# Kernel tuning notes

Hardware: AMD Instinct MI355X
Metric: run time of the kernel (lower is better)

Reference implementation:

```python
import jax, jax.numpy as jnp
import numpy as np

NUM_FEATURES = 256   # 2**8
BOND_DIM = 16
N_CORES = 8          # log2(NUM_FEATURES)
BATCH = 262144


def _mpo_cores(mpo_weights, n, bond_dim):
    # Slice the flat parameter vector into n cores of shape (l, r, 2, 2).
    shapes = [(1, bond_dim, 2, 2)] + [(bond_dim, bond_dim, 2, 2)] * (n - 2) + [(bond_dim, 1, 2, 2)]
    cores, off = [], 0
    for s in shapes:
        sz = int(np.prod(s))
        cores.append(mpo_weights[off:off + sz].reshape(s))
        off += sz
    return cores


def _contract_mpo(cores):
    # Sequentially contract the tensor-train cores into the full (2^n, 2^n) matrix.
    # T has axes (bond, I, J) where I/J accumulate the row/col physical bits
    # in order i1..in / j1..jn, matching the original einsum + reshape.
    T = cores[0][0]          # (r, 2, 2)
    dim = 2
    for A in cores[1:]:      # A: (l, r2, 2, 2)
        T = jnp.einsum('aIJ,abkm->bIkJm', T, A).reshape(A.shape[1], dim * 2, dim * 2)
        dim *= 2
    return T[0]              # (2^n, 2^n)


def setup_inputs() -> dict:
    key = jax.random.key(0)
    k1, k2, k3 = jax.random.split(key, 3)
    total = 2 * 4 * BOND_DIM + (N_CORES - 2) * 4 * BOND_DIM ** 2  # 6272
    return {
        'x': jax.random.normal(k1, (BATCH, NUM_FEATURES), dtype=jnp.float32),
        'mpo_weights': jax.random.normal(k2, (total,), dtype=jnp.float32) * 0.1,
        'dense_kernel': jax.random.normal(k3, (NUM_FEATURES, 1), dtype=jnp.float32) * 0.1,
        'dense_bias': jnp.zeros((1,), dtype=jnp.float32),
    }


def reference(x, mpo_weights, dense_kernel, dense_bias):
    W = _contract_mpo(_mpo_cores(mpo_weights, N_CORES, BOND_DIM))  # (256, 256)
    h = jnp.square(x @ W)                                          # (B, 256)
    return h @ dense_kernel + dense_bias                           # (B, 1)
```

## Files before the change

kernel.cpp:

```cpp
#include <hip/hip_runtime.h>
#include <hip/hip_bf16.h>

typedef _Float16 half8 __attribute__((ext_vector_type(8)));
typedef float    floatx4 __attribute__((ext_vector_type(4)));

#define WSCALE      4096.0f
#define WSCALE_INV  (1.0f/(4096.0f*4096.0f))

#define T1_OFF   0
#define U_OFF    4096
#define WF16_OFF 8192

__global__ __launch_bounds__(256)
void mpo_prep1(const float* __restrict__ w, float* __restrict__ ws) {
    __shared__ __align__(16) float wL[3136];
    __shared__ __align__(16) float sL[4352];
    const int tid = threadIdx.x;

    {
        const floatx4* s4 = reinterpret_cast<const floatx4*>(w + blockIdx.x * 3136);
        floatx4* d4 = reinterpret_cast<floatx4*>(wL);
        for (int i = tid; i < 784; i += 256) d4[i] = s4[i];
    }
    __syncthreads();

    if (blockIdx.x == 0) {
        {
            int li = tid;
            int mm = li & 3, kk = (li >> 2) & 3, c = li >> 4;
            int k1 = kk >> 1, k2 = kk & 1, m1 = mm >> 1, m2 = mm & 1;
            float s = 0.f;
#pragma unroll
            for (int b = 0; b < 16; ++b)
                s += wL[b * 4 + k1 * 2 + m1] * wL[64 + b * 64 + c * 4 + k2 * 2 + m2];
            sL[li] = s;
        }
        {
            const int i0 = (tid >> 4) * 4, j0 = (tid & 15) * 4;
            const float* Ab = wL + 1088 + (i0 >> 2) * 64;
            const float* Bb = wL + 2112 + j0;
            float acc[4][4] = {};
#pragma unroll
            for (int b = 0; b < 16; ++b) {
                floatx4 ar = *reinterpret_cast<const floatx4*>(Ab + b * 4);
                floatx4 br = *reinterpret_cast<const floatx4*>(Bb + b * 64);
#pragma unroll
                for (int r = 0; r < 4; ++r)
#pragma unroll
                    for (int s = 0; s < 4; ++s) acc[r][s] += ar[r] * br[s];
            }
#pragma unroll
            for (int r = 0; r < 4; ++r)
#pragma unroll
            for (int s = 0; s < 4; ++s) {
                int i = i0 + r, j = j0 + s;
                sL[256 + (i >> 2) * 256 + (j >> 2) * 16 +
                   ((i >> 1) & 1) * 8 + ((j >> 1) & 1) * 4 + (i & 1) * 2 + (j & 1)] = acc[r][s];
            }
        }
        __syncthreads();
        {
            const int p0 = (tid >> 6) * 4, q0 = (tid & 63) * 4;
            float acc[4][4] = {};
#pragma unroll
            for (int a = 0; a < 16; ++a) {
                floatx4 pr = *reinterpret_cast<const floatx4*>(sL + a * 16 + p0);
                floatx4 qr = *reinterpret_cast<const floatx4*>(sL + 256 + a * 256 + q0);
#pragma unroll
                for (int r = 0; r < 4; ++r)
#pragma unroll
                    for (int s = 0; s < 4; ++s) acc[r][s] += pr[r] * qr[s];
            }
#pragma unroll
            for (int r = 0; r < 4; ++r)
#pragma unroll
            for (int s = 0; s < 4; ++s) {
                int p = p0 + r, q = q0 + s;
                ws[T1_OFF + (q >> 4) * 256 + ((p >> 2) * 4 + ((q >> 2) & 3)) * 16 +
                   (p & 3) * 4 + (q & 3)] = acc[r][s];
            }
        }
    } else {
        {
            const int i0 = (tid >> 4) * 4, j0 = (tid & 15) * 4;
            const float* Ab = wL + (i0 >> 2) * 64;
            const float* Bb = wL + 1024 + j0;
            float acc[4][4] = {};
#pragma unroll
            for (int b = 0; b < 16; ++b) {
                floatx4 ar = *reinterpret_cast<const floatx4*>(Ab + b * 4);
                floatx4 br = *reinterpret_cast<const floatx4*>(Bb + b * 64);
#pragma unroll
                for (int r = 0; r < 4; ++r)
#pragma unroll
                    for (int s = 0; s < 4; ++s) acc[r][s] += ar[r] * br[s];
            }
#pragma unroll
            for (int r = 0; r < 4; ++r)
#pragma unroll
            for (int s = 0; s < 4; ++s) {
                int i = i0 + r, j = j0 + s;
                sL[(i >> 2) * 256 + (j >> 2) * 16 +
                   ((i >> 1) & 1) * 8 + ((j >> 1) & 1) * 4 + (i & 1) * 2 + (j & 1)] = acc[r][s];
            }
        }
        {
            int li = tid;
            int mm = li & 3, kk = (li >> 2) & 3, a = li >> 4;
            int k1 = kk >> 1, k2 = kk & 1, m1 = mm >> 1, m2 = mm & 1;
            float s = 0.f;
#pragma unroll
            for (int b = 0; b < 16; ++b)
                s += wL[2048 + a * 64 + b * 4 + k1 * 2 + m1] * wL[3072 + b * 4 + k2 * 2 + m2];
            sL[4096 + li] = s;
        }
        __syncthreads();
        {
            const int r0 = (tid >> 2) * 4, q0 = (tid & 3) * 4;
            float acc[4][4] = {};
#pragma unroll
            for (int b = 0; b < 16; ++b) {
                floatx4 ar = *reinterpret_cast<const floatx4*>(sL + (r0 >> 4) * 256 + b * 16 + (r0 & 15));
                floatx4 br = *reinterpret_cast<const floatx4*>(sL + 4096 + b * 16 + q0);
#pragma unroll
                for (int r = 0; r < 4; ++r)
#pragma unroll
                    for (int s = 0; s < 4; ++s) acc[r][s] += ar[r] * br[s];
            }
#pragma unroll
            for (int r = 0; r < 4; ++r)
#pragma unroll
            for (int s = 0; s < 4; ++s)
                ws[U_OFF + (r0 + r) * 16 + q0 + s] = acc[r][s];
        }
    }
}

__global__ __launch_bounds__(256)
void mpo_prep2(const float* __restrict__ ws, _Float16* __restrict__ Wf) {
    int idx = blockIdx.x * blockDim.x + threadIdx.x;
    int J4 = idx & 255, I4 = idx >> 8;
    int I16 = I4 >> 4, kc = (I4 >> 2) & 3, k2 = I4 & 3;
    int J16 = J4 >> 4, mc = (J4 >> 2) & 3, m2 = J4 & 3;
    const float* T1 = ws + T1_OFF;
    const float* U  = ws + U_OFF + (((kc * 4 + mc) * 4 + k2) * 4 + m2);
    float s = 0.f;
#pragma unroll
    for (int a = 0; a < 16; ++a)
        s += T1[(a * 16 + I16) * 16 + J16] * U[a * 256];
    int n = J4 >> 4, lr = J4 & 15, kk = I4 >> 5, gg = (I4 >> 3) & 3, j = I4 & 7;
    Wf[(((n * 8 + kk) * 64) + gg * 16 + lr) * 8 + j] = (_Float16)(s * WSCALE);
}

__global__ __launch_bounds__(512, 2)
void mpo_main(const float* __restrict__ x, const _Float16* __restrict__ Wf,
              const float* __restrict__ dk, const float* __restrict__ bias,
              float* __restrict__ out) {
    extern __shared__ _Float16 Wl[];
    float* dkL = reinterpret_cast<float*>(Wl + 65536);

    const int tid  = threadIdx.x;
    const int lane = tid & 63;
    const int wave = tid >> 6;
    const int lrow = lane & 15;
    const int g    = lane >> 4;

    const long blockbase = (long)blockIdx.x * 1024;
    const float* xb = x + (blockbase + wave * 32 + lrow) * 256 + g * 8;
    const int PASS_STRIDE = 256 * 256;
    const int SET_STRIDE  = 16 * 256;

    half8 a0[8], a1[8];
    floatx4 lo[8], hi[8];

#define SB()  __builtin_amdgcn_sched_barrier(0)
#define XLD(i, xn) do { const float* p_ = (xn) + (i) * 32;              \
                     lo[i] = *reinterpret_cast<const floatx4*>(p_);     \
                     hi[i] = *reinterpret_cast<const floatx4*>(p_ + 4); } while (0)
#define XLD_ALL(xn) do { XLD(0,xn); XLD(1,xn); XLD(2,xn); XLD(3,xn); \
                         XLD(4,xn); XLD(5,xn); XLD(6,xn); XLD(7,xn); } while (0)
#define XCVT(dst, i) do { half8 f_;                                           \
                     f_[0] = (_Float16)lo[i][0]; f_[1] = (_Float16)lo[i][1];  \
                     f_[2] = (_Float16)lo[i][2]; f_[3] = (_Float16)lo[i][3];  \
                     f_[4] = (_Float16)hi[i][0]; f_[5] = (_Float16)hi[i][1];  \
                     f_[6] = (_Float16)hi[i][2]; f_[7] = (_Float16)hi[i][3];  \
                     dst[i] = f_; } while (0)
#define XCVT_ALL(dst) do { XCVT(dst,0); XCVT(dst,1); XCVT(dst,2); XCVT(dst,3); \
                           XCVT(dst,4); XCVT(dst,5); XCVT(dst,6); XCVT(dst,7); } while (0)

    XLD_ALL(xb);
    SB();
    {
        const floatx4* src = reinterpret_cast<const floatx4*>(Wf);
        floatx4* dst = reinterpret_cast<floatx4*>(Wl);
#pragma unroll
        for (int i = 0; i < 16; ++i)
            dst[tid + i * 512] = src[tid + i * 512];
    }
    if (tid < 256) dkL[tid] = dk[tid];
    const float bs = bias[0];
    __syncthreads();
    XCVT_ALL(a0);
    XLD_ALL(xb + SET_STRIDE);
    SB();
    XCVT_ALL(a1);
    SB();

    const half8* Wv = reinterpret_cast<const half8*>(Wl);

#pragma unroll 1
    for (int p = 0; p < 4; ++p) {
        if (p < 3) { XLD_ALL(xb + (p + 1) * PASS_STRIDE); }
        SB();

        float rp0[4] = {0, 0, 0, 0}, rp1[4] = {0, 0, 0, 0};
#pragma unroll 1
        for (int n = 0; n < 16; ++n) {
            const float kv = dkL[n * 16 + lrow];
            const half8* Wn = Wv + n * 512 + lane;
            floatx4 c0 = {0, 0, 0, 0}, c1 = {0, 0, 0, 0};
#pragma unroll
            for (int kk = 0; kk < 8; ++kk) {
                half8 b = Wn[kk * 64];
                c0 = __builtin_amdgcn_mfma_f32_16x16x32_f16(a0[kk], b, c0, 0, 0, 0);
                c1 = __builtin_amdgcn_mfma_f32_16x16x32_f16(a1[kk], b, c1, 0, 0, 0);
            }
#pragma unroll
            for (int r = 0; r < 4; ++r) {
                rp0[r] += c0[r] * c0[r] * kv;
                rp1[r] += c1[r] * c1[r] * kv;
            }
        }

        if (p < 3) {
            XCVT_ALL(a0);
            XLD_ALL(xb + (p + 1) * PASS_STRIDE + SET_STRIDE);
        }
        SB();

#pragma unroll
        for (int r = 0; r < 4; ++r) {
            float v0 = rp0[r], v1 = rp1[r];
            v0 += __shfl_xor(v0, 1); v1 += __shfl_xor(v1, 1);
            v0 += __shfl_xor(v0, 2); v1 += __shfl_xor(v1, 2);
            v0 += __shfl_xor(v0, 4); v1 += __shfl_xor(v1, 4);
            v0 += __shfl_xor(v0, 8); v1 += __shfl_xor(v1, 8);
            rp0[r] = v0; rp1[r] = v1;
        }
        if (lrow == 0) {
            floatx4 o0, o1;
#pragma unroll
            for (int r = 0; r < 4; ++r) {
                o0[r] = rp0[r] * WSCALE_INV + bs;
                o1[r] = rp1[r] * WSCALE_INV + bs;
            }
            float* ob = out + blockbase + p * 256 + wave * 32 + g * 4;
            *reinterpret_cast<floatx4*>(ob)      = o0;
            *reinterpret_cast<floatx4*>(ob + 16) = o1;
        }

        if (p < 3) { XCVT_ALL(a1); }
        SB();
    }
}

extern "C" void kernel_launch(void* const* d_in, const int* in_sizes, int n_in,
                              void* d_out, int out_size, void* d_ws, size_t ws_size,
                              hipStream_t stream) {
    const float* x    = (const float*)d_in[0];
    const float* w    = (const float*)d_in[1];
    const float* dk   = (const float*)d_in[2];
    const float* bias = (const float*)d_in[3];
    float* out = (float*)d_out;
    float* ws  = (float*)d_ws;

    _Float16* Wf16 = (_Float16*)(ws + WF16_OFF);

    static bool attr_set = false;
    if (!attr_set) {
        hipFuncSetAttribute((const void*)mpo_main,
                            hipFuncAttributeMaxDynamicSharedMemorySize, 132096);
        attr_set = true;
    }

    mpo_prep1<<<2, 256, 0, stream>>>(w, ws);
    mpo_prep2<<<256, 256, 0, stream>>>(ws, Wf16);

    mpo_main<<<256, 512, 132096, stream>>>(x, Wf16, dk, bias, out);
}
```

Before: 63.78 us.

## Fuse MPO prep kernels and process one 16-row set per wave per step

```diff
diff --git a/kernel.cpp b/kernel.cpp
--- a/kernel.cpp
+++ b/kernel.cpp
@@ -7,149 +7,145 @@
 #define WSCALE      4096.0f
 #define WSCALE_INV  (1.0f/(4096.0f*4096.0f))
 
-#define T1_OFF   0
-#define U_OFF    4096
 #define WF16_OFF 8192
 
 __global__ __launch_bounds__(256)
-void mpo_prep1(const float* __restrict__ w, float* __restrict__ ws) {
-    __shared__ __align__(16) float wL[3136];
-    __shared__ __align__(16) float sL[4352];
+void mpo_prep(const float* __restrict__ w, _Float16* __restrict__ Wf) {
+    __shared__ __align__(16) float wL[6272];
+    __shared__ __align__(16) float sL[8704];
+    __shared__ __align__(16) float tuL[8192];
     const int tid = threadIdx.x;
 
     {
-        const floatx4* s4 = reinterpret_cast<const floatx4*>(w + blockIdx.x * 3136);
+        const floatx4* s4 = reinterpret_cast<const floatx4*>(w);
         floatx4* d4 = reinterpret_cast<floatx4*>(wL);
-        for (int i = tid; i < 784; i += 256) d4[i] = s4[i];
-    }
-    __syncthreads();
-
-    if (blockIdx.x == 0) {
-        {
-            int li = tid;
-            int mm = li & 3, kk = (li >> 2) & 3, c = li >> 4;
-            int k1 = kk >> 1, k2 = kk & 1, m1 = mm >> 1, m2 = mm & 1;
-            float s = 0.f;
-#pragma unroll
-            for (int b = 0; b < 16; ++b)
-                s += wL[b * 4 + k1 * 2 + m1] * wL[64 + b * 64 + c * 4 + k2 * 2 + m2];
-            sL[li] = s;
-        }
-        {
-            const int i0 = (tid >> 4) * 4, j0 = (tid & 15) * 4;
-            const float* Ab = wL + 1088 + (i0 >> 2) * 64;
-            const float* Bb = wL + 2112 + j0;
-            float acc[4][4] = {};
-#pragma unroll
-            for (int b = 0; b < 16; ++b) {
-                floatx4 ar = *reinterpret_cast<const floatx4*>(Ab + b * 4);
-                floatx4 br = *reinterpret_cast<const floatx4*>(Bb + b * 64);
-#pragma unroll
-                for (int r = 0; r < 4; ++r)
-#pragma unroll
-                    for (int s = 0; s < 4; ++s) acc[r][s] += ar[r] * br[s];
-            }
-#pragma unroll
-            for (int r = 0; r < 4; ++r)
-#pragma unroll
-            for (int s = 0; s < 4; ++s) {
-                int i = i0 + r, j = j0 + s;
-                sL[256 + (i >> 2) * 256 + (j >> 2) * 16 +
-                   ((i >> 1) & 1) * 8 + ((j >> 1) & 1) * 4 + (i & 1) * 2 + (j & 1)] = acc[r][s];
-            }
-        }
-        __syncthreads();
-        {
-            const int p0 = (tid >> 6) * 4, q0 = (tid & 63) * 4;
-            float acc[4][4] = {};
-#pragma unroll
-            for (int a = 0; a < 16; ++a) {
-                floatx4 pr = *reinterpret_cast<const floatx4*>(sL + a * 16 + p0);
-                floatx4 qr = *reinterpret_cast<const floatx4*>(sL + 256 + a * 256 + q0);
-#pragma unroll
-                for (int r = 0; r < 4; ++r)
-#pragma unroll
-                    for (int s = 0; s < 4; ++s) acc[r][s] += pr[r] * qr[s];
-            }
-#pragma unroll
-            for (int r = 0; r < 4; ++r)
-#pragma unroll
-            for (int s = 0; s < 4; ++s) {
-                int p = p0 + r, q = q0 + s;
-                ws[T1_OFF + (q >> 4) * 256 + ((p >> 2) * 4 + ((q >> 2) & 3)) * 16 +
-                   (p & 3) * 4 + (q & 3)] = acc[r][s];
-            }
-        }
-    } else {
-        {
-            const int i0 = (tid >> 4) * 4, j0 = (tid & 15) * 4;
-            const float* Ab = wL + (i0 >> 2) * 64;
-            const float* Bb = wL + 1024 + j0;
-            float acc[4][4] = {};
-#pragma unroll
-            for (int b = 0; b < 16; ++b) {
-                floatx4 ar = *reinterpret_cast<const floatx4*>(Ab + b * 4);
-                floatx4 br = *reinterpret_cast<const floatx4*>(Bb + b * 64);
-#pragma unroll
-                for (int r = 0; r < 4; ++r)
-#pragma unroll
-                    for (int s = 0; s < 4; ++s) acc[r][s] += ar[r] * br[s];
-            }
-#pragma unroll
-            for (int r = 0; r < 4; ++r)
-#pragma unroll
-            for (int s = 0; s < 4; ++s) {
-                int i = i0 + r, j = j0 + s;
-                sL[(i >> 2) * 256 + (j >> 2) * 16 +
-                   ((i >> 1) & 1) * 8 + ((j >> 1) & 1) * 4 + (i & 1) * 2 + (j & 1)] = acc[r][s];
-            }
-        }
-        {
-            int li = tid;
-            int mm = li & 3, kk = (li >> 2) & 3, a = li >> 4;
-            int k1 = kk >> 1, k2 = kk & 1, m1 = mm >> 1, m2 = mm & 1;
-            float s = 0.f;
-#pragma unroll
-            for (int b = 0; b < 16; ++b)
-                s += wL[2048 + a * 64 + b * 4 + k1 * 2 + m1] * wL[3072 + b * 4 + k2 * 2 + m2];
-            sL[4096 + li] = s;
-        }
-        __syncthreads();
-        {
-            const int r0 = (tid >> 2) * 4, q0 = (tid & 3) * 4;
-            float acc[4][4] = {};
-#pragma unroll
-            for (int b = 0; b < 16; ++b) {
-                floatx4 ar = *reinterpret_cast<const floatx4*>(sL + (r0 >> 4) * 256 + b * 16 + (r0 & 15));
-                floatx4 br = *reinterpret_cast<const floatx4*>(sL + 4096 + b * 16 + q0);
-#pragma unroll
-                for (int r = 0; r < 4; ++r)
-#pragma unroll
-                    for (int s = 0; s < 4; ++s) acc[r][s] += ar[r] * br[s];
-            }
-#pragma unroll
-            for (int r = 0; r < 4; ++r)
-#pragma unroll
-            for (int s = 0; s < 4; ++s)
-                ws[U_OFF + (r0 + r) * 16 + q0 + s] = acc[r][s];
-        }
-    }
-}
-
-__global__ __launch_bounds__(256)
-void mpo_prep2(const float* __restrict__ ws, _Float16* __restrict__ Wf) {
-    int idx = blockIdx.x * blockDim.x + threadIdx.x;
-    int J4 = idx & 255, I4 = idx >> 8;
-    int I16 = I4 >> 4, kc = (I4 >> 2) & 3, k2 = I4 & 3;
-    int J16 = J4 >> 4, mc = (J4 >> 2) & 3, m2 = J4 & 3;
-    const float* T1 = ws + T1_OFF;
-    const float* U  = ws + U_OFF + (((kc * 4 + mc) * 4 + k2) * 4 + m2);
-    float s = 0.f;
-#pragma unroll
-    for (int a = 0; a < 16; ++a)
-        s += T1[(a * 16 + I16) * 16 + J16] * U[a * 256];
-    int n = J4 >> 4, lr = J4 & 15, kk = I4 >> 5, gg = (I4 >> 3) & 3, j = I4 & 7;
-    Wf[(((n * 8 + kk) * 64) + gg * 16 + lr) * 8 + j] = (_Float16)(s * WSCALE);
+        for (int i = tid; i < 1568; i += 256) d4[i] = s4[i];
+    }
+    __syncthreads();
+
+    {
+        int li = tid;
+        int mm = li & 3, kk = (li >> 2) & 3, c = li >> 4;
+        int k1 = kk >> 1, k2 = kk & 1, m1 = mm >> 1, m2 = mm & 1;
+        float s = 0.f;
+#pragma unroll
+        for (int b = 0; b < 16; ++b)
+            s += wL[b * 4 + k1 * 2 + m1] * wL[64 + b * 64 + c * 4 + k2 * 2 + m2];
+        sL[li] = s;
+    }
+    {
+        const int i0 = (tid >> 4) * 4, j0 = (tid & 15) * 4;
+        const float* Ab = wL + 1088 + (i0 >> 2) * 64;
+        const float* Bb = wL + 2112 + j0;
+        float acc[4][4] = {};
+#pragma unroll
+        for (int b = 0; b < 16; ++b) {
+            floatx4 ar = *reinterpret_cast<const floatx4*>(Ab + b * 4);
+            floatx4 br = *reinterpret_cast<const floatx4*>(Bb + b * 64);
+#pragma unroll
+            for (int r = 0; r < 4; ++r)
+#pragma unroll
+                for (int s = 0; s < 4; ++s) acc[r][s] += ar[r] * br[s];
+        }
+#pragma unroll
+        for (int r = 0; r < 4; ++r)
+#pragma unroll
+        for (int s = 0; s < 4; ++s) {
+            int i = i0 + r, j = j0 + s;
+            sL[256 + (i >> 2) * 256 + (j >> 2) * 16 +
+               ((i >> 1) & 1) * 8 + ((j >> 1) & 1) * 4 + (i & 1) * 2 + (j & 1)] = acc[r][s];
+        }
+    }
+    {
+        const int i0 = (tid >> 4) * 4, j0 = (tid & 15) * 4;
+        const float* Ab = wL + 3136 + (i0 >> 2) * 64;
+        const float* Bb = wL + 4160 + j0;
+        float acc[4][4] = {};
+#pragma unroll
+        for (int b = 0; b < 16; ++b) {
+            floatx4 ar = *reinterpret_cast<const floatx4*>(Ab + b * 4);
+            floatx4 br = *reinterpret_cast<const floatx4*>(Bb + b * 64);
+#pragma unroll
+            for (int r = 0; r < 4; ++r)
+#pragma unroll
+                for (int s = 0; s < 4; ++s) acc[r][s] += ar[r] * br[s];
+        }
+#pragma unroll
+        for (int r = 0; r < 4; ++r)
+#pragma unroll
+        for (int s = 0; s < 4; ++s) {
+            int i = i0 + r, j = j0 + s;
+            sL[4352 + (i >> 2) * 256 + (j >> 2) * 16 +
+               ((i >> 1) & 1) * 8 + ((j >> 1) & 1) * 4 + (i & 1) * 2 + (j & 1)] = acc[r][s];
+        }
+    }
+    {
+        int li = tid;
+        int mm = li & 3, kk = (li >> 2) & 3, a = li >> 4;
+        int k1 = kk >> 1, k2 = kk & 1, m1 = mm >> 1, m2 = mm & 1;
+        float s = 0.f;
+#pragma unroll
+        for (int b = 0; b < 16; ++b)
+            s += wL[5184 + a * 64 + b * 4 + k1 * 2 + m1] * wL[6208 + b * 4 + k2 * 2 + m2];
+        sL[8448 + li] = s;
+    }
+    __syncthreads();
+
+    {
+        const int p0 = (tid >> 6) * 4, q0 = (tid & 63) * 4;
+        float acc[4][4] = {};
+#pragma unroll
+        for (int a = 0; a < 16; ++a) {
+            floatx4 pr = *reinterpret_cast<const floatx4*>(sL + a * 16 + p0);
+            floatx4 qr = *reinterpret_cast<const floatx4*>(sL + 256 + a * 256 + q0);
+#pragma unroll
+            for (int r = 0; r < 4; ++r)
+#pragma unroll
+                for (int s = 0; s < 4; ++s) acc[r][s] += pr[r] * qr[s];
+        }
+#pragma unroll
+        for (int r = 0; r < 4; ++r)
+#pragma unroll
+        for (int s = 0; s < 4; ++s) {
+            int p = p0 + r, q = q0 + s;
+            tuL[(q >> 4) * 256 + ((p >> 2) * 4 + ((q >> 2) & 3)) * 16 +
+                (p & 3) * 4 + (q & 3)] = acc[r][s];
+        }
+    }
+    {
+        const int r0 = (tid >> 2) * 4, q0 = (tid & 3) * 4;
+        float acc[4][4] = {};
+#pragma unroll
+        for (int b = 0; b < 16; ++b) {
+            floatx4 ar = *reinterpret_cast<const floatx4*>(sL + 4352 + (r0 >> 4) * 256 + b * 16 + (r0 & 15));
+            floatx4 br = *reinterpret_cast<const floatx4*>(sL + 8448 + b * 16 + q0);
+#pragma unroll
+            for (int r = 0; r < 4; ++r)
+#pragma unroll
+                for (int s = 0; s < 4; ++s) acc[r][s] += ar[r] * br[s];
+        }
+#pragma unroll
+        for (int r = 0; r < 4; ++r)
+#pragma unroll
+        for (int s = 0; s < 4; ++s)
+            tuL[4096 + (r0 + r) * 16 + q0 + s] = acc[r][s];
+    }
+    __syncthreads();
+
+    {
+        int idx = blockIdx.x * 256 + tid;
+        int J4 = idx & 255, I4 = idx >> 8;
+        int I16 = I4 >> 4, kc = (I4 >> 2) & 3, k2v = I4 & 3;
+        int mc = (J4 >> 2) & 3, m2v = J4 & 3;
+        int J16 = J4 >> 4;
+        const float* Uc = tuL + 4096 + (((kc * 4 + mc) * 4 + k2v) * 4 + m2v);
+        float s = 0.f;
+#pragma unroll
+        for (int a = 0; a < 16; ++a)
+            s += tuL[(a * 16 + I16) * 16 + J16] * Uc[a * 256];
+        int nn = J4 >> 4, lr = J4 & 15, kq = I4 >> 5, gg = (I4 >> 3) & 3, jj = I4 & 7;
+        Wf[(((nn * 8 + kq) * 64) + gg * 16 + lr) * 8 + jj] = (_Float16)(s * WSCALE);
+    }
 }
 
 __global__ __launch_bounds__(512, 2)
@@ -166,11 +162,10 @@
     const int g    = lane >> 4;
 
     const long blockbase = (long)blockIdx.x * 1024;
-    const float* xb = x + (blockbase + wave * 32 + lrow) * 256 + g * 8;
-    const int PASS_STRIDE = 256 * 256;
-    const int SET_STRIDE  = 16 * 256;
-
-    half8 a0[8], a1[8];
+    const float* xb = x + (blockbase + wave * 16 + lrow) * 256 + g * 8;
+    const int SET_STRIDE = 128 * 256;
+
+    half8 a[8];
     floatx4 lo[8], hi[8];
 
 #define SB()  __builtin_amdgcn_sched_barrier(0)
@@ -179,14 +174,14 @@
                      hi[i] = *reinterpret_cast<const floatx4*>(p_ + 4); } while (0)
 #define XLD_ALL(xn) do { XLD(0,xn); XLD(1,xn); XLD(2,xn); XLD(3,xn); \
                          XLD(4,xn); XLD(5,xn); XLD(6,xn); XLD(7,xn); } while (0)
-#define XCVT(dst, i) do { half8 f_;                                           \
+#define XCVT(i) do { half8 f_;                                                \
                      f_[0] = (_Float16)lo[i][0]; f_[1] = (_Float16)lo[i][1];  \
                      f_[2] = (_Float16)lo[i][2]; f_[3] = (_Float16)lo[i][3];  \
                      f_[4] = (_Float16)hi[i][0]; f_[5] = (_Float16)hi[i][1];  \
                      f_[6] = (_Float16)hi[i][2]; f_[7] = (_Float16)hi[i][3];  \
-                     dst[i] = f_; } while (0)
-#define XCVT_ALL(dst) do { XCVT(dst,0); XCVT(dst,1); XCVT(dst,2); XCVT(dst,3); \
-                           XCVT(dst,4); XCVT(dst,5); XCVT(dst,6); XCVT(dst,7); } while (0)
+                     a[i] = f_; } while (0)
+#define XCVT_ALL() do { XCVT(0); XCVT(1); XCVT(2); XCVT(3); \
+                        XCVT(4); XCVT(5); XCVT(6); XCVT(7); } while (0)
 
     XLD_ALL(xb);
     SB();
@@ -200,66 +195,52 @@
     if (tid < 256) dkL[tid] = dk[tid];
     const float bs = bias[0];
     __syncthreads();
-    XCVT_ALL(a0);
+
+    float kreg[16];
+#pragma unroll
+    for (int n = 0; n < 16; ++n) kreg[n] = dkL[n * 16 + lrow];
+
+    XCVT_ALL();
     XLD_ALL(xb + SET_STRIDE);
     SB();
-    XCVT_ALL(a1);
-    SB();
 
     const half8* Wv = reinterpret_cast<const half8*>(Wl);
 
 #pragma unroll 1
-    for (int p = 0; p < 4; ++p) {
-        if (p < 3) { XLD_ALL(xb + (p + 1) * PASS_STRIDE); }
-        SB();
-
-        float rp0[4] = {0, 0, 0, 0}, rp1[4] = {0, 0, 0, 0};
+    for (int s = 0; s < 8; ++s) {
+        float rp[4] = {0, 0, 0, 0};
 #pragma unroll 1
         for (int n = 0; n < 16; ++n) {
-            const float kv = dkL[n * 16 + lrow];
             const half8* Wn = Wv + n * 512 + lane;
-            floatx4 c0 = {0, 0, 0, 0}, c1 = {0, 0, 0, 0};
-#pragma unroll
-            for (int kk = 0; kk < 8; ++kk) {
-                half8 b = Wn[kk * 64];
-                c0 = __builtin_amdgcn_mfma_f32_16x16x32_f16(a0[kk], b, c0, 0, 0, 0);
-                c1 = __builtin_amdgcn_mfma_f32_16x16x32_f16(a1[kk], b, c1, 0, 0, 0);
-            }
-#pragma unroll
-            for (int r = 0; r < 4; ++r) {
-                rp0[r] += c0[r] * c0[r] * kv;
-                rp1[r] += c1[r] * c1[r] * kv;
-            }
-        }
-
-        if (p < 3) {
-            XCVT_ALL(a0);
-            XLD_ALL(xb + (p + 1) * PASS_STRIDE + SET_STRIDE);
-        }
+            floatx4 c0 = {0, 0, 0, 0};
+#pragma unroll
+            for (int kk = 0; kk < 8; ++kk)
+                c0 = __builtin_amdgcn_mfma_f32_16x16x32_f16(a[kk], Wn[kk * 64], c0, 0, 0, 0);
+            const float kv = kreg[n];
+#pragma unroll
+            for (int r = 0; r < 4; ++r)
+                rp[r] += c0[r] * c0[r] * kv;
+        }
+
+        if (s < 7) { XCVT_ALL(); }
+        if (s < 6) { XLD_ALL(xb + (s + 2) * SET_STRIDE); }
         SB();
 
 #pragma unroll
         for (int r = 0; r < 4; ++r) {
-            float v0 = rp0[r], v1 = rp1[r];
-            v0 += __shfl_xor(v0, 1); v1 += __shfl_xor(v1, 1);
-            v0 += __shfl_xor(v0, 2); v1 += __shfl_xor(v1, 2);
-            v0 += __shfl_xor(v0, 4); v1 += __shfl_xor(v1, 4);
-            v0 += __shfl_xor(v0, 8); v1 += __shfl_xor(v1, 8);
-            rp0[r] = v0; rp1[r] = v1;
+            float v = rp[r];
+            v += __shfl_xor(v, 1);
+            v += __shfl_xor(v, 2);
+            v += __shfl_xor(v, 4);
+            v += __shfl_xor(v, 8);
+            rp[r] = v;
         }
         if (lrow == 0) {
-            floatx4 o0, o1;
-#pragma unroll
-            for (int r = 0; r < 4; ++r) {
-                o0[r] = rp0[r] * WSCALE_INV + bs;
-                o1[r] = rp1[r] * WSCALE_INV + bs;
-            }
-            float* ob = out + blockbase + p * 256 + wave * 32 + g * 4;
-            *reinterpret_cast<floatx4*>(ob)      = o0;
-            *reinterpret_cast<floatx4*>(ob + 16) = o1;
-        }
-
-        if (p < 3) { XCVT_ALL(a1); }
+            floatx4 o;
+#pragma unroll
+            for (int r = 0; r < 4; ++r) o[r] = rp[r] * WSCALE_INV + bs;
+            *reinterpret_cast<floatx4*>(out + blockbase + s * 128 + wave * 16 + g * 4) = o;
+        }
         SB();
     }
 }
@@ -283,8 +264,7 @@
         attr_set = true;
     }
 
-    mpo_prep1<<<2, 256, 0, stream>>>(w, ws);
-    mpo_prep2<<<256, 256, 0, stream>>>(ws, Wf16);
+    mpo_prep<<<256, 256, 0, stream>>>(w, Wf16);
 
     mpo_main<<<256, 512, 132096, stream>>>(x, Wf16, dk, bias, out);
 }
```

Result: no change. 62.60 us, median of 3 (-1.8%).
